# Kernel tuning notes

Hardware: AMD Instinct MI355X
Metric: run time of the kernel (lower is better)

Reference implementation:

```python
import jax, jax.numpy as jnp
import numpy as np

B = 64
BAND = 16384
N_OSC = 32
CH = 64
T_IN = 32
N_NOISE_FRAMES = BAND // 4          # 4096
NOISE_STEP = BAND // N_NOISE_FRAMES  # 4 samples per noise frame
NOISE_COEFFS = NOISE_STEP // 2 + 1   # 3 rfft coefficients
N_UP = int(np.log2(N_NOISE_FRAMES) - np.log2(T_IN))  # 7 doubling blocks
LOWEST_FREQ = 20.0 / 11025.0


def _conv1d(x, w, b, pad):
    # x: (B, Cin, T), w: (Cout, Cin, K)
    out = jax.lax.conv_general_dilated(x, w, (1,), [(pad, pad)],
                                       dimension_numbers=('NCH', 'OIH', 'NCH'))
    return out + b[None, :, None]


def _leaky(x):
    return jnp.where(x > 0, x, 0.2 * x)


def _lin_interp(x, size):
    # torch F.interpolate(mode='linear', align_corners=False) along last axis
    n = x.shape[-1]
    coords = (jnp.arange(size, dtype=jnp.float32) + 0.5) * (n / size) - 0.5
    coords = jnp.clip(coords, 0.0, n - 1.0)
    lo = jnp.floor(coords).astype(jnp.int32)
    hi = jnp.minimum(lo + 1, n - 1)
    frac = (coords - lo.astype(jnp.float32)).astype(x.dtype)
    return x[..., lo] * (1.0 - frac) + x[..., hi] * frac


def setup_inputs() -> dict:
    key = jax.random.key(0)
    ks = jax.random.split(key, 16)
    s = 0.1
    return {
        'x': jax.random.normal(ks[0], (B, T_IN, CH), jnp.float32),
        'noise': jax.random.uniform(ks[1], (B, N_NOISE_FRAMES, NOISE_STEP), jnp.float32, -1.0, 1.0),
        'net_w': jax.random.normal(ks[2], (4, CH, CH, 3), jnp.float32) * s,
        'net_b': jax.random.normal(ks[3], (4, CH), jnp.float32) * s,
        'final_w': jax.random.normal(ks[4], (CH, CH, 3), jnp.float32) * s,
        'final_b': jax.random.normal(ks[5], (CH,), jnp.float32) * s,
        'amp_w': jax.random.normal(ks[6], (N_OSC, CH), jnp.float32) * s,
        'amp_b': jax.random.normal(ks[7], (N_OSC,), jnp.float32) * s,
        'freq_w': jax.random.normal(ks[8], (N_OSC, CH), jnp.float32) * s,
        'freq_b': jax.random.normal(ks[9], (N_OSC,), jnp.float32) * s,
        'nz_init_w': jax.random.normal(ks[10], (CH, CH), jnp.float32) * s,
        'nz_init_b': jax.random.normal(ks[11], (CH,), jnp.float32) * s,
        'nz_up_w': jax.random.normal(ks[12], (N_UP, CH, CH, 3), jnp.float32) * s,
        'nz_up_b': jax.random.normal(ks[13], (N_UP, CH), jnp.float32) * s,
        'nz_final_w': jax.random.normal(ks[14], (NOISE_COEFFS, CH), jnp.float32) * s,
        'nz_final_b': jax.random.normal(ks[15], (NOISE_COEFFS,), jnp.float32) * s,
    }


def reference(x, noise, net_w, net_b, final_w, final_b, amp_w, amp_b, freq_w, freq_b,
              nz_init_w, nz_init_b, nz_up_w, nz_up_b, nz_final_w, nz_final_b):
    z = jnp.transpose(x, (0, 2, 1))  # (B, CH, T_IN)
    for i in range(4):
        z = _leaky(_conv1d(z, net_w[i], net_b[i], 1))
    z = _conv1d(z, final_w, final_b, 1)

    # --- OscillatorBank: sigmoid freq (constrained), abs amp, linear upsample,
    # phase accumulation via cumsum, summed sinusoids ---
    amp = jnp.abs(jnp.einsum('bct,oc->bot', z, amp_w) + amp_b[None, :, None])
    freq = jax.nn.sigmoid(jnp.einsum('bct,oc->bot', z, freq_w) + freq_b[None, :, None])
    freq = LOWEST_FREQ + freq * (1.0 - LOWEST_FREQ)
    amp = _lin_interp(amp, BAND)    # (B, N_OSC, BAND)
    freq = _lin_interp(freq, BAND)  # (B, N_OSC, BAND)
    phase = jnp.cumsum(freq * jnp.pi, axis=-1)
    harm = jnp.sum(amp * jnp.sin(phase), axis=1, keepdims=True)  # (B, 1, BAND)

    # 1x1 conv to rfft coeffs, squared, applied per-frame to uniform noise ---
    y = jnp.einsum('bct,oc->bot', z, nz_init_w) + nz_init_b[None, :, None]
    for i in range(N_UP):
        y = jnp.repeat(y, 2, axis=-1)
        y = _leaky(_conv1d(y, nz_up_w[i], nz_up_b[i], 1))
    coeffs = jnp.einsum('bct,oc->bot', y, nz_final_w) + nz_final_b[None, :, None]
    coeffs = coeffs ** 2                      # squared=True, activation=identity
    coeffs = jnp.transpose(coeffs, (0, 2, 1))  # (B, frames, NOISE_COEFFS)
    spec = jnp.fft.rfft(noise, axis=-1, norm='ortho')   # (B, frames, NOISE_COEFFS)
    filt = spec * coeffs.astype(spec.dtype)
    nz = jnp.fft.irfft(filt, n=NOISE_STEP, axis=-1, norm='ortho')  # (B, frames, step)
    nz = nz.reshape(B, 1, BAND)

    return harm + nz
```

## Files before the change

kernel.cpp:

```cpp
#include <hip/hip_runtime.h>
#include <math.h>

#define LOWEST_FREQ_F 0.00181405895691609977f

typedef short bf16x8 __attribute__((ext_vector_type(8)));
typedef float f32x16 __attribute__((ext_vector_type(16)));

__device__ __forceinline__ float lrelu(float x) { return x > 0.f ? x : 0.2f * x; }
__device__ __forceinline__ float sin_rev(float fr) { return __builtin_amdgcn_sinf(fr); }
__device__ __forceinline__ float bf2f(unsigned short u) {
  union { unsigned int i; float f; } x; x.i = ((unsigned int)u) << 16; return x.f;
}
__device__ __forceinline__ unsigned short f2bf(float f) {
  union { float f; unsigned int i; } x; x.f = f;
  unsigned int r = x.i + 0x7FFFu + ((x.i >> 16) & 1u);
  return (unsigned short)(r >> 16);
}
__device__ __forceinline__ unsigned int pack2(float a, float b) {
  return (unsigned int)f2bf(a) | ((unsigned int)f2bf(b) << 16);
}

__global__ __launch_bounds__(256) void prep_kernel(
    const float* __restrict__ net_w, const float* __restrict__ fin_w,
    const float* __restrict__ amp_w, const float* __restrict__ frq_w,
    const float* __restrict__ nzi_w, const float* __restrict__ nzu_w,
    float* __restrict__ wtF4, float* __restrict__ awfwT,
    float* __restrict__ nzT, short* __restrict__ wfold)
{
  int idx = blockIdx.x * 256 + threadIdx.x;
  if (idx < 20480) {
    int l = idx >> 12, r = idx & 4095;
    int ci = r >> 6, co = r & 63;
    const float* src = (l < 4) ? (net_w + l * 12288) : fin_w;
    const float* wb = src + co * 192 + ci * 3;
    float4 v = make_float4(wb[0], wb[1], wb[2], 0.f);
    ((float4*)wtF4)[idx] = v;
  } else if (idx < 24576) {
    int r = idx - 20480;
    int c2 = r >> 7, rem = r & 127, o = rem >> 2, k = rem & 3;
    int c = c2 * 2 + (k >> 1);
    awfwT[r] = (k & 1) ? frq_w[o * 64 + c] : amp_w[o * 64 + c];
  } else if (idx < 28672) {
    int r = idx - 24576; int c = r >> 6, o = r & 63;
    nzT[r] = nzi_w[o * 64 + c];
  } else if (idx < 28672 + 114688) {
    int r = idx - 28672;
    int l = r >> 14, q = r & 16383;
    int pd = q >> 12, co = (q >> 6) & 63, ci = q & 63;
    const float* wb = nzu_w + l * 12288 + co * 192 + ci * 3;
    float v;
    if      (pd == 0) v = wb[0];
    else if (pd == 1) v = wb[1] + wb[2];
    else if (pd == 2) v = wb[0] + wb[1];
    else              v = wb[2];
    wfold[r] = (short)f2bf(v);
  }
}

template<int TIN>
__device__ __forceinline__ void noise_layer(
    const short* tin, short* tout, const short* __restrict__ wf,
    const float* __restrict__ bias, int tid)
{
  const int L  = tid & 63;
  const int w  = tid >> 6;
  const int mt = w & 1;
  const int ng = w >> 1;

  bf16x8 Af[4][4];
  {
    const short* wb = wf + (mt*32 + (L & 31))*64 + ((L >> 5) << 3);
    #pragma unroll
    for (int pd = 0; pd < 4; ++pd)
      #pragma unroll
      for (int ks = 0; ks < 4; ++ks)
        Af[pd][ks] = *(const bf16x8*)(wb + pd*4096 + ks*16);
  }
  f32x16 binit;
  #pragma unroll
  for (int r = 0; r < 16; ++r)
    binit[r] = bias[mt*32 + (r & 3) + 8*(r >> 2) + 4*(L >> 5)];

  if (tid < 64) { tout[tid] = 0; tout[(2*TIN + 1)*72 + tid] = 0; }

  constexpr int TOT = TIN / 32;
  constexpr int NPG = (TOT + 3) / 4;
  #pragma unroll
  for (int nt = 0; nt < NPG; ++nt) {
    int ntile = ng*NPG + nt;
    if (ntile < TOT) {
      int s = ntile*32 + (L & 31);
      const short* bp = tin + s*72 + ((L >> 5) << 3);
      f32x16 Ce = binit, Co = binit;
      #pragma unroll
      for (int ks = 0; ks < 4; ++ks) {
        bf16x8 Bm = *(const bf16x8*)(bp + ks*16);
        bf16x8 B0 = *(const bf16x8*)(bp + 72 + ks*16);
        bf16x8 Bp = *(const bf16x8*)(bp + 144 + ks*16);
        Ce = __builtin_amdgcn_mfma_f32_32x32x16_bf16(Af[0][ks], Bm, Ce, 0, 0, 0);
        Ce = __builtin_amdgcn_mfma_f32_32x32x16_bf16(Af[1][ks], B0, Ce, 0, 0, 0);
        Co = __builtin_amdgcn_mfma_f32_32x32x16_bf16(Af[2][ks], B0, Co, 0, 0, 0);
        Co = __builtin_amdgcn_mfma_f32_32x32x16_bf16(Af[3][ks], Bp, Co, 0, 0, 0);
      }
      #pragma unroll
      for (int q4 = 0; q4 < 4; ++q4) {
        int co0 = mt*32 + 8*q4 + 4*(L >> 5);
        uint2 ve, vo;
        ve.x = pack2(lrelu(Ce[4*q4+0]), lrelu(Ce[4*q4+1]));
        ve.y = pack2(lrelu(Ce[4*q4+2]), lrelu(Ce[4*q4+3]));
        vo.x = pack2(lrelu(Co[4*q4+0]), lrelu(Co[4*q4+1]));
        vo.y = pack2(lrelu(Co[4*q4+2]), lrelu(Co[4*q4+3]));
        *(uint2*)&tout[(2*s + 1)*72 + co0] = ve;
        *(uint2*)&tout[(2*s + 2)*72 + co0] = vo;
      }
    }
  }
  __syncthreads();
}

template<int NT, int ROFF, bool TOGLOBAL>
__device__ __forceinline__ void up_stage(
    const short* bin, short* bout, unsigned short* gout,
    const short* __restrict__ wf, const float* __restrict__ bias, int tid)
{
  const int L  = tid & 63;
  const int w  = tid >> 6;
  const int mt = w & 1;
  const int pg = w >> 1;

  bf16x8 Af[4][4];
  {
    const short* wb = wf + (mt*32 + (L & 31))*64 + ((L >> 5) << 3);
    #pragma unroll
    for (int pd = 0; pd < 4; ++pd)
      #pragma unroll
      for (int ks = 0; ks < 4; ++ks)
        Af[pd][ks] = *(const bf16x8*)(wb + pd*4096 + ks*16);
  }
  f32x16 binit;
  #pragma unroll
  for (int r = 0; r < 16; ++r)
    binit[r] = bias[mt*32 + (r & 3) + 8*(r >> 2) + 4*(L >> 5)];

  for (int n = pg; n < NT; n += 2) {
    int sl = n*32 + (L & 31);
    const short* bp = bin + (sl + ROFF)*72 + ((L >> 5) << 3);
    f32x16 Ce = binit, Co = binit;
    #pragma unroll
    for (int ks = 0; ks < 4; ++ks) {
      bf16x8 Bm = *(const bf16x8*)(bp + ks*16);
      bf16x8 B0 = *(const bf16x8*)(bp + 72 + ks*16);
      bf16x8 Bp = *(const bf16x8*)(bp + 144 + ks*16);
      Ce = __builtin_amdgcn_mfma_f32_32x32x16_bf16(Af[0][ks], Bm, Ce, 0, 0, 0);
      Ce = __builtin_amdgcn_mfma_f32_32x32x16_bf16(Af[1][ks], B0, Ce, 0, 0, 0);
      Co = __builtin_amdgcn_mfma_f32_32x32x16_bf16(Af[2][ks], B0, Co, 0, 0, 0);
      Co = __builtin_amdgcn_mfma_f32_32x32x16_bf16(Af[3][ks], Bp, Co, 0, 0, 0);
    }
    #pragma unroll
    for (int q4 = 0; q4 < 4; ++q4) {
      int co0 = mt*32 + 8*q4 + 4*(L >> 5);
      uint2 ve, vo;
      ve.x = pack2(lrelu(Ce[4*q4+0]), lrelu(Ce[4*q4+1]));
      ve.y = pack2(lrelu(Ce[4*q4+2]), lrelu(Ce[4*q4+3]));
      vo.x = pack2(lrelu(Co[4*q4+0]), lrelu(Co[4*q4+1]));
      vo.y = pack2(lrelu(Co[4*q4+2]), lrelu(Co[4*q4+3]));
      if (TOGLOBAL) {
        *(uint2*)(gout + (size_t)(2*sl)*64 + co0)     = ve;
        *(uint2*)(gout + (size_t)(2*sl + 1)*64 + co0) = vo;
      } else {
        *(uint2*)&bout[(2*sl)*72 + co0]     = ve;
        *(uint2*)&bout[(2*sl + 1)*72 + co0] = vo;
      }
    }
  }
}

__global__ __launch_bounds__(256) void up345(
    const unsigned short* __restrict__ y3, unsigned short* __restrict__ y6,
    const short* __restrict__ wfold, const float* __restrict__ nzu_b)
{
  __shared__ __align__(16) short s3[66*72];
  __shared__ __align__(16) short s4[128*72];
  __shared__ __align__(16) short s5[192*72];

  const int b   = blockIdx.y;
  const int bx  = blockIdx.x;
  const int tid = threadIdx.x;

  const unsigned short* inb = y3 + (size_t)b * 256 * 64;
  for (int c = tid; c < 66*8; c += 256) {
    int row = c >> 3, pos = (c & 7) << 3;
    int g = 32*bx - 2 + row;
    bf16x8 v = {0,0,0,0,0,0,0,0};
    if (g >= 0 && g < 256) v = *(const bf16x8*)(inb + (size_t)g*64 + pos);
    *(bf16x8*)&s3[row*72 + pos] = v;
  }
  __syncthreads();

  up_stage<2,0,false>(s3, s4, nullptr, wfold + 3*16384, nzu_b + 3*64, tid);
  __syncthreads();
  if (bx == 0) {
    if (tid < 128) s4[(tid >> 6)*72 + (tid & 63)] = 0;
  } else if (bx == 7) {
    for (int i = tid; i < 62*64; i += 256) {
      int r = 66 + (i >> 6);
      s4[r*72 + (i & 63)] = 0;
    }
  }
  __syncthreads();

  up_stage<3,0,false>(s4, s5, nullptr, wfold + 4*16384, nzu_b + 4*64, tid);
  __syncthreads();
  if (bx == 0) {
    if (tid < 128) s5[(tid >> 6)*72 + (tid & 63)] = 0;
  } else if (bx == 7) {
    for (int i = tid; i < 62*64; i += 256) {
      int r = 130 + (i >> 6);
      s5[r*72 + (i & 63)] = 0;
    }
  }
  __syncthreads();

  unsigned short* outb = y6 + ((size_t)b*2048 + 256*bx) * 64;
  up_stage<4,1,true>(s5, nullptr, outb, wfold + 5*16384, nzu_b + 5*64, tid);
}

__global__ __launch_bounds__(512) void z_front(
    const float* __restrict__ x, const float* __restrict__ wtF4,
    const float* __restrict__ net_b, const float* __restrict__ fin_b,
    const float* __restrict__ awfwT, const float* __restrict__ amp_b,
    const float* __restrict__ frq_b,
    const float* __restrict__ nzT, const float* __restrict__ nzi_b,
    const short* __restrict__ wfold, const float* __restrict__ nzu_b,
    unsigned short* __restrict__ y3, float* __restrict__ amp_o,
    float* __restrict__ frq_o, float* __restrict__ ph_o)
{
  __shared__ __align__(16) char arena[86976];
  short* tileB = (short*)arena;
  short* tileA = (short*)(arena + 37152);
  float* za    = (float*)(arena + 55872);
  float* zb    = (float*)(arena + 65088);
  float* zt    = (float*)(arena + 74304);
  float* fl    = (float*)(arena + 82752);

  const int b   = blockIdx.x;
  const int tid = threadIdx.x;
  const int co  = tid & 63;
  const int wv  = tid >> 6;

  for (int idx = tid; idx < 2048; idx += 512) {
    int t = idx >> 6, c = idx & 63;
    za[c*36 + t + 1] = x[b*2048 + idx];
  }
  if (tid < 64) {
    za[tid*36] = 0.f; za[tid*36 + 33] = 0.f;
    zb[tid*36] = 0.f; zb[tid*36 + 33] = 0.f;
  }
  __syncthreads();

  float* pa = za;
  float* pb = zb;
  for (int l = 0; l < 5; ++l) {
    {
      const int t0 = wv << 2;
      float bv = (l < 4) ? net_b[l*64 + co] : fin_b[co];
      float acc[4];
      #pragma unroll
      for (int j = 0; j < 4; ++j) acc[j] = bv;

      const float4* wp = ((const float4*)wtF4) + l*4096 + co;
      float4 wCur[8], wNxt[8];
      #pragma unroll
      for (int k = 0; k < 8; ++k) wCur[k] = wp[k*64];

      for (int cc = 0; cc < 8; ++cc) {
        if (cc < 7) {
          #pragma unroll
          for (int k = 0; k < 8; ++k) wNxt[k] = wp[((cc+1)*8 + k)*64];
        }
        #pragma unroll
        for (int k = 0; k < 8; ++k) {
          const int ci = cc*8 + k;
          const float* rowp = pa + ci*36 + t0;
          float4 zA = *(const float4*)(rowp);
          float2 zB = *(const float2*)(rowp + 4);
          float rr[6] = {zA.x, zA.y, zA.z, zA.w, zB.x, zB.y};
          float4 wgt = wCur[k];
          #pragma unroll
          for (int j = 0; j < 4; ++j) {
            acc[j] = fmaf(wgt.x, rr[j],   acc[j]);
            acc[j] = fmaf(wgt.y, rr[j+1], acc[j]);
            acc[j] = fmaf(wgt.z, rr[j+2], acc[j]);
          }
        }
        if (cc < 7) {
          #pragma unroll
          for (int k = 0; k < 8; ++k) wCur[k] = wNxt[k];
        }
      }

      if (l < 4) {
        #pragma unroll
        for (int j = 0; j < 4; ++j)
          pb[co*36 + t0 + j + 1] = lrelu(acc[j]);
      } else {
        #pragma unroll
        for (int j = 0; j < 4; ++j) {
          int t = t0 + j;
          pb[co*36 + t] = acc[j];
          zt[t*66 + co] = acc[j];
        }
      }
    }
    __syncthreads();
    float* tp = pa; pa = pb; pb = tp;
  }
  const float* zf = pa;

  {
    const int q = wv;
    float bv0 = nzi_b[co];
    float acc[4];
    #pragma unroll
    for (int j = 0; j < 4; ++j) acc[j] = bv0;
    #pragma unroll 8
    for (int c = 0; c < 64; ++c) {
      float4 zv = *(const float4*)(zf + c*36 + (q << 2));
      float wvv = nzT[c*64 + co];
      acc[0] = fmaf(wvv, zv.x, acc[0]);
      acc[1] = fmaf(wvv, zv.y, acc[1]);
      acc[2] = fmaf(wvv, zv.z, acc[2]);
      acc[3] = fmaf(wvv, zv.w, acc[3]);
    }
    #pragma unroll
    for (int j = 0; j < 4; ++j)
      tileA[((q << 2) + j + 1)*72 + co] = (short)f2bf(acc[j]);
  }
  if (tid < 64) { tileA[tid] = 0; tileA[33*72 + tid] = 0; }

  #pragma unroll
  for (int tt = 0; tt < 2; ++tt) {
    int task = tid + 512*tt;
    int o = task & 31, t = task >> 5;
    float aa = amp_b[o], ff = frq_b[o];
    #pragma unroll 8
    for (int c2 = 0; c2 < 32; ++c2) {
      float4 w4 = ((const float4*)awfwT)[c2*32 + o];
      float2 zv = *(const float2*)(zt + t*66 + c2*2);
      aa = fmaf(w4.x, zv.x, aa); ff = fmaf(w4.y, zv.x, ff);
      aa = fmaf(w4.z, zv.y, aa); ff = fmaf(w4.w, zv.y, ff);
    }
    aa = fabsf(aa);
    float sg = 1.f / (1.f + expf(-ff));
    float fq = LOWEST_FREQ_F + sg * (1.f - LOWEST_FREQ_F);
    amp_o[b*1024 + o*32 + t] = aa;
    frq_o[b*1024 + o*32 + t] = fq;
    fl[o*33 + t] = fq;
  }
  __syncthreads();

  if (wv == 7 && (tid & 63) < 32) {
    const int o = tid & 31;
    double P = 256.0 * (double)fl[o*33];
    double hd = P * 0.5;
    ph_o[b*1024 + o*32] = (float)(hd - floor(hd));
    for (int i = 1; i < 32; ++i) {
      P += 256.0 * ((double)fl[o*33 + i - 1] + (double)fl[o*33 + i]);
      hd = P * 0.5;
      ph_o[b*1024 + o*32 + i] = (float)(hd - floor(hd));
    }
  }

  noise_layer<32> (tileA, tileB, wfold + 0*16384, nzu_b + 0*64, tid);
  noise_layer<64> (tileB, tileA, wfold + 1*16384, nzu_b + 1*64, tid);
  noise_layer<128>(tileA, tileB, wfold + 2*16384, nzu_b + 2*64, tid);

  unsigned short* yb = y3 + (size_t)b * 16384;
  for (int c = tid; c < 2048; c += 512) {
    int row = c >> 3, pos = (c & 7) << 3;
    *(bf16x8*)(yb + c*8) = *(const bf16x8*)&tileB[(row + 1)*72 + pos];
  }
}

__global__ __launch_bounds__(256) void final_fused(
    const unsigned short* __restrict__ in,
    const short* __restrict__ wf, const float* __restrict__ bias,
    const float* __restrict__ nzf_w, const float* __restrict__ nzf_b,
    const float* __restrict__ noise,
    const float* __restrict__ amp, const float* __restrict__ frq,
    const float* __restrict__ ph, float* __restrict__ out)
{
  constexpr int STILE = 128, Tin = 2048, ROWS = STILE + 2, G = STILE / 64;
  __shared__ __align__(16) short lB[ROWS * 72];
  __shared__ __align__(16) short yT[256 * 72];
  __shared__ float al[1024], fqv[1024], pl[1024];
  __shared__ float wl[192];

  const int b   = blockIdx.y;
  const int s0  = blockIdx.x * STILE;
  const int tid = threadIdx.x;
  const int L   = tid & 63;
  const int w   = tid >> 6;
  const int mt  = w & 1;
  const int ng  = w >> 1;

  for (int i = tid; i < 1024; i += 256) {
    al[i]  = amp[b*1024 + i];
    fqv[i] = frq[b*1024 + i];
    pl[i]  = ph[b*1024 + i];
  }
  if (tid < 192) { int o = tid >> 6, c = tid & 63; wl[c*3 + o] = nzf_w[tid]; }

  bf16x8 Af[4][4];
  {
    const short* wb = wf + (mt*32 + (L & 31))*64 + ((L >> 5) << 3);
    #pragma unroll
    for (int pd = 0; pd < 4; ++pd)
      #pragma unroll
      for (int ks = 0; ks < 4; ++ks)
        Af[pd][ks] = *(const bf16x8*)(wb + pd*4096 + ks*16);
  }

  const unsigned short* inb = in + (size_t)b * Tin * 64;
  for (int c = tid; c < ROWS*8; c += 256) {
    int row = c >> 3, pos = (c & 7) << 3;
    int g = s0 - 1 + row;
    bf16x8 v = {0,0,0,0,0,0,0,0};
    if (g >= 0 && g < Tin) v = *(const bf16x8*)(inb + (size_t)g*64 + pos);
    *(bf16x8*)&lB[row*72 + pos] = v;
  }

  f32x16 binit;
  #pragma unroll
  for (int r = 0; r < 16; ++r)
    binit[r] = bias[mt*32 + (r & 3) + 8*(r >> 2) + 4*(L >> 5)];

  __syncthreads();

  #pragma unroll
  for (int nt = 0; nt < G; ++nt) {
    int s_loc = ng*(32*G) + nt*32 + (L & 31);
    const short* bp = lB + s_loc*72 + ((L >> 5) << 3);
    f32x16 Ce = binit, Co = binit;
    #pragma unroll
    for (int ks = 0; ks < 4; ++ks) {
      bf16x8 Bm = *(const bf16x8*)(bp + ks*16);
      bf16x8 B0 = *(const bf16x8*)(bp + 72 + ks*16);
      bf16x8 Bp = *(const bf16x8*)(bp + 144 + ks*16);
      Ce = __builtin_amdgcn_mfma_f32_32x32x16_bf16(Af[0][ks], Bm, Ce, 0, 0, 0);
      Ce = __builtin_amdgcn_mfma_f32_32x32x16_bf16(Af[1][ks], B0, Ce, 0, 0, 0);
      Co = __builtin_amdgcn_mfma_f32_32x32x16_bf16(Af[2][ks], B0, Co, 0, 0, 0);
      Co = __builtin_amdgcn_mfma_f32_32x32x16_bf16(Af[3][ks], Bp, Co, 0, 0, 0);
    }
    #pragma unroll
    for (int q4 = 0; q4 < 4; ++q4) {
      int co0 = mt*32 + 8*q4 + 4*(L >> 5);
      uint2 ve, vo;
      ve.x = pack2(lrelu(Ce[4*q4+0]), lrelu(Ce[4*q4+1]));
      ve.y = pack2(lrelu(Ce[4*q4+2]), lrelu(Ce[4*q4+3]));
      vo.x = pack2(lrelu(Co[4*q4+0]), lrelu(Co[4*q4+1]));
      vo.y = pack2(lrelu(Co[4*q4+2]), lrelu(Co[4*q4+3]));
      *(uint2*)&yT[(2*s_loc)*72 + co0]     = ve;
      *(uint2*)&yT[(2*s_loc + 1)*72 + co0] = vo;
    }
  }
  __syncthreads();

  {
    const short* yr = &yT[tid * 72];
    float c0 = nzf_b[0], c1 = nzf_b[1], c2 = nzf_b[2];
    #pragma unroll
    for (int c8 = 0; c8 < 8; ++c8) {
      bf16x8 v = *(const bf16x8*)(yr + c8*8);
      #pragma unroll
      for (int j = 0; j < 8; ++j) {
        float yv = bf2f((unsigned short)v[j]);
        int c = c8*8 + j;
        c0 = fmaf(wl[c*3+0], yv, c0);
        c1 = fmaf(wl[c*3+1], yv, c1);
        c2 = fmaf(wl[c*3+2], yv, c2);
      }
    }
    c0 *= c0; c1 *= c1; c2 *= c2;

    const int fb = 2*s0 + tid;
    const float4 n = *(const float4*)(noise + ((size_t)b*4096 + fb)*4);
    float F0  = c0 * (n.x + n.y + n.z + n.w) * 0.5f;
    float F1r = c1 * (n.x - n.z) * 0.5f;
    float F1i = -(c1 * (n.y - n.w) * 0.5f);
    float F2  = c2 * (n.x - n.y + n.z - n.w) * 0.5f;
    float r0 = 0.5f * (F0 + 2.f*F1r + F2);
    float r1 = 0.5f * (F0 - 2.f*F1i - F2);
    float r2 = 0.5f * (F0 - 2.f*F1r + F2);
    float r3 = 0.5f * (F0 + 2.f*F1i - F2);

    const int t0 = fb * 4;
    float s0a = 0.f, s1a = 0.f, s2a = 0.f, s3a = 0.f;
    if (t0 < 256) {
      const float tp = (float)(t0 + 1) * 0.5f;
      #pragma unroll 4
      for (int o = 0; o < 32; ++o) {
        float f0 = fqv[o*32], am = al[o*32];
        float hf = 0.5f * f0;
        float v0 = tp * f0, v1 = v0 + hf, v2 = v1 + hf, v3 = v2 + hf;
        s0a += am * sin_rev(v0 - floorf(v0));
        s1a += am * sin_rev(v1 - floorf(v1));
        s2a += am * sin_rev(v2 - floorf(v2));
        s3a += am * sin_rev(v3 - floorf(v3));
      }
    } else if (t0 >= 16128) {
      const float tp = (float)(t0 - 16127) * 0.5f;
      #pragma unroll 4
      for (int o = 0; o < 32; ++o) {
        float f0 = fqv[o*32 + 31], am = al[o*32 + 31], p = pl[o*32 + 31];
        float hf = 0.5f * f0;
        float v0 = p + tp * f0, v1 = v0 + hf, v2 = v1 + hf, v3 = v2 + hf;
        s0a += am * sin_rev(v0 - floorf(v0));
        s1a += am * sin_rev(v1 - floorf(v1));
        s2a += am * sin_rev(v2 - floorf(v2));
        s3a += am * sin_rev(v3 - floorf(v3));
      }
    } else {
      const int i  = (t0 - 256) >> 9;
      const int m0 = (t0 - 256) & 511;
      float mm[4], fa[4], mq[4];
      #pragma unroll
      for (int js = 0; js < 4; ++js) {
        float mmv = (float)(m0 + 1 + js);
        mm[js] = mmv;
        fa[js] = ((float)(m0 + js) + 0.5f) * (1.f/512.f);
        mq[js] = mmv * mmv * (1.f/1024.f);
      }
      #pragma unroll 4
      for (int o = 0; o < 32; ++o) {
        float f0 = fqv[o*32 + i], f1 = fqv[o*32 + i + 1];
        float a0 = al[o*32 + i],  a1 = al[o*32 + i + 1];
        float p  = pl[o*32 + i];
        float df = f1 - f0, da = a1 - a0;
        #pragma unroll
        for (int js = 0; js < 4; ++js) {
          float av   = fmaf(da, fa[js], a0);
          float part = fmaf(df, mq[js], mm[js] * f0);
          float v    = fmaf(part, 0.5f, p);
          float fr   = v - floorf(v);
          float sv   = av * sin_rev(fr);
          if      (js == 0) s0a += sv;
          else if (js == 1) s1a += sv;
          else if (js == 2) s2a += sv;
          else              s3a += sv;
        }
      }
    }
    float4 res = make_float4(s0a + r0, s1a + r1, s2a + r2, s3a + r3);
    *(float4*)(out + ((size_t)b*4096 + fb)*4) = res;
  }
}

extern "C" void kernel_launch(void* const* d_in, const int* in_sizes, int n_in,
                              void* d_out, int out_size, void* d_ws, size_t ws_size,
                              hipStream_t stream) {
  (void)in_sizes; (void)n_in; (void)out_size; (void)ws_size;
  const float* x     = (const float*)d_in[0];
  const float* noise = (const float*)d_in[1];
  const float* net_w = (const float*)d_in[2];
  const float* net_b = (const float*)d_in[3];
  const float* fin_w = (const float*)d_in[4];
  const float* fin_b = (const float*)d_in[5];
  const float* amp_w = (const float*)d_in[6];
  const float* amp_b = (const float*)d_in[7];
  const float* frq_w = (const float*)d_in[8];
  const float* frq_b = (const float*)d_in[9];
  const float* nzi_w = (const float*)d_in[10];
  const float* nzi_b = (const float*)d_in[11];
  const float* nzu_w = (const float*)d_in[12];
  const float* nzu_b = (const float*)d_in[13];
  const float* nzf_w = (const float*)d_in[14];
  const float* nzf_b = (const float*)d_in[15];
  float* out = (float*)d_out;

  short* y3    = (short*)d_ws;
  short* y6    = y3 + (size_t)64*256*64;
  short* wfold = y6 + (size_t)64*2048*64;
  float* wtF4  = (float*)(wfold + 7*16384);
  float* awfwT = wtF4 + 81920;
  float* nzT   = awfwT + 4096;
  float* ampv  = nzT + 4096;
  float* frqv  = ampv + 65536;
  float* phv   = frqv + 65536;

  prep_kernel<<<dim3(560), dim3(256), 0, stream>>>(
      net_w, fin_w, amp_w, frq_w, nzi_w, nzu_w, wtF4, awfwT, nzT, wfold);

  z_front<<<dim3(64), dim3(512), 0, stream>>>(
      x, wtF4, net_b, fin_b, awfwT, amp_b, frq_b, nzT, nzi_b,
      wfold, nzu_b, (unsigned short*)y3, ampv, frqv, phv);

  up345<<<dim3(8, 64), dim3(256), 0, stream>>>(
      (unsigned short*)y3, (unsigned short*)y6, wfold, nzu_b);

  final_fused<<<dim3(16, 64), dim3(256), 0, stream>>>(
      (unsigned short*)y6, wfold + 6*16384, nzu_b + 6*64,
      nzf_w, nzf_b, noise, ampv, frqv, phv, out);
}
```

Baseline: 204.7 us.

## Double z_front threads and split conv input channels across waves

z_front now launches 1024 threads per block instead of 512. The five conv layers are restructured so that each thread handles one time step and 8 output channels over a slice of input channels. Partial sums are reduced with a cross-half shuffle plus an LDS scratch buffer and an extra barrier. The noise init, amp/freq projection and noise_layer tile distribution (NPG halved) are adjusted to the larger block, aiming to cut the latency of this 64-block, underoccupied kernel at the cost of more LDS, reduction overhead and register pressure under 1024-thread bounds.

```diff
diff --git a/kernel.cpp b/kernel.cpp
--- a/kernel.cpp
+++ b/kernel.cpp
@@ -84,7 +84,7 @@
   if (tid < 64) { tout[tid] = 0; tout[(2*TIN + 1)*72 + tid] = 0; }
 
   constexpr int TOT = TIN / 32;
-  constexpr int NPG = (TOT + 3) / 4;
+  constexpr int NPG = (TOT + 7) / 8;
   #pragma unroll
   for (int nt = 0; nt < NPG; ++nt) {
     int ntile = ng*NPG + nt;
@@ -225,7 +225,7 @@
   up_stage<4,1,true>(s5, nullptr, outb, wfold + 5*16384, nzu_b + 5*64, tid);
 }
 
-__global__ __launch_bounds__(512) void z_front(
+__global__ __launch_bounds__(1024) void z_front(
     const float* __restrict__ x, const float* __restrict__ wtF4,
     const float* __restrict__ net_b, const float* __restrict__ fin_b,
     const float* __restrict__ awfwT, const float* __restrict__ amp_b,
@@ -235,20 +235,21 @@
     unsigned short* __restrict__ y3, float* __restrict__ amp_o,
     float* __restrict__ frq_o, float* __restrict__ ph_o)
 {
-  __shared__ __align__(16) char arena[86976];
+  __shared__ __align__(16) char arena[95168];
   short* tileB = (short*)arena;
   short* tileA = (short*)(arena + 37152);
   float* za    = (float*)(arena + 55872);
   float* zb    = (float*)(arena + 65088);
   float* zt    = (float*)(arena + 74304);
   float* fl    = (float*)(arena + 82752);
+  float* sc    = (float*)(arena + 86976);
 
   const int b   = blockIdx.x;
   const int tid = threadIdx.x;
   const int co  = tid & 63;
   const int wv  = tid >> 6;
 
-  for (int idx = tid; idx < 2048; idx += 512) {
+  for (int idx = tid; idx < 2048; idx += 1024) {
     int t = idx >> 6, c = idx & 63;
     za[c*36 + t + 1] = x[b*2048 + idx];
   }
@@ -258,57 +259,81 @@
   }
   __syncthreads();
 
+  const int L    = tid & 63;
+  const int t    = L & 31;
+  const int half = L >> 5;
+  const int co8  = wv & 7;
+  const int ciq  = wv >> 3;
+
   float* pa = za;
   float* pb = zb;
   for (int l = 0; l < 5; ++l) {
+    float acc[8];
+    if (ciq == 0 && half == 0) {
+      const float* bp = (l < 4) ? (net_b + l*64) : fin_b;
+      #pragma unroll
+      for (int j = 0; j < 8; ++j) acc[j] = bp[co8*8 + j];
+    } else {
+      #pragma unroll
+      for (int j = 0; j < 8; ++j) acc[j] = 0.f;
+    }
+
+    const float4* wp = ((const float4*)wtF4) + l*4096 + co8*8;
+    const int ci0 = ciq*32 + half;
+
+    float4 wc[8];
+    float zc0, zc1, zc2;
     {
-      const int t0 = wv << 2;
-      float bv = (l < 4) ? net_b[l*64 + co] : fin_b[co];
-      float acc[4];
-      #pragma unroll
-      for (int j = 0; j < 4; ++j) acc[j] = bv;
-
-      const float4* wp = ((const float4*)wtF4) + l*4096 + co;
-      float4 wCur[8], wNxt[8];
-      #pragma unroll
-      for (int k = 0; k < 8; ++k) wCur[k] = wp[k*64];
-
-      for (int cc = 0; cc < 8; ++cc) {
-        if (cc < 7) {
-          #pragma unroll
-          for (int k = 0; k < 8; ++k) wNxt[k] = wp[((cc+1)*8 + k)*64];
-        }
+      const float* zr = pa + ci0*36 + t;
+      zc0 = zr[0]; zc1 = zr[1]; zc2 = zr[2];
+      #pragma unroll
+      for (int j = 0; j < 8; ++j) wc[j] = wp[ci0*64 + j];
+    }
+    #pragma unroll
+    for (int s = 0; s < 16; ++s) {
+      float4 wn[8];
+      float zn0 = 0.f, zn1 = 0.f, zn2 = 0.f;
+      if (s < 15) {
+        int ci = ci0 + 2*(s + 1);
+        const float* zr = pa + ci*36 + t;
+        zn0 = zr[0]; zn1 = zr[1]; zn2 = zr[2];
         #pragma unroll
-        for (int k = 0; k < 8; ++k) {
-          const int ci = cc*8 + k;
-          const float* rowp = pa + ci*36 + t0;
-          float4 zA = *(const float4*)(rowp);
-          float2 zB = *(const float2*)(rowp + 4);
-          float rr[6] = {zA.x, zA.y, zA.z, zA.w, zB.x, zB.y};
-          float4 wgt = wCur[k];
-          #pragma unroll
-          for (int j = 0; j < 4; ++j) {
-            acc[j] = fmaf(wgt.x, rr[j],   acc[j]);
-            acc[j] = fmaf(wgt.y, rr[j+1], acc[j]);
-            acc[j] = fmaf(wgt.z, rr[j+2], acc[j]);
-          }
-        }
-        if (cc < 7) {
-          #pragma unroll
-          for (int k = 0; k < 8; ++k) wCur[k] = wNxt[k];
-        }
-      }
-
-      if (l < 4) {
+        for (int j = 0; j < 8; ++j) wn[j] = wp[ci*64 + j];
+      }
+      #pragma unroll
+      for (int j = 0; j < 8; ++j) {
+        acc[j] = fmaf(wc[j].x, zc0, acc[j]);
+        acc[j] = fmaf(wc[j].y, zc1, acc[j]);
+        acc[j] = fmaf(wc[j].z, zc2, acc[j]);
+      }
+      if (s < 15) {
+        zc0 = zn0; zc1 = zn1; zc2 = zn2;
         #pragma unroll
-        for (int j = 0; j < 4; ++j)
-          pb[co*36 + t0 + j + 1] = lrelu(acc[j]);
-      } else {
-        #pragma unroll
-        for (int j = 0; j < 4; ++j) {
-          int t = t0 + j;
-          pb[co*36 + t] = acc[j];
-          zt[t*66 + co] = acc[j];
+        for (int j = 0; j < 8; ++j) wc[j] = wn[j];
+      }
+    }
+    #pragma unroll
+    for (int j = 0; j < 8; ++j) acc[j] += __shfl_xor(acc[j], 32, 64);
+
+    if (ciq == 1) {
+      #pragma unroll
+      for (int jj = 0; jj < 4; ++jj) {
+        int j = half*4 + jj;
+        sc[(co8*8 + j)*32 + t] = acc[j];
+      }
+    }
+    __syncthreads();
+    if (ciq == 0) {
+      #pragma unroll
+      for (int jj = 0; jj < 4; ++jj) {
+        int j = half*4 + jj;
+        int c = co8*8 + j;
+        float v = acc[j] + sc[c*32 + t];
+        if (l < 4) {
+          pb[c*36 + t + 1] = lrelu(v);
+        } else {
+          pb[c*36 + t] = v;
+          zt[t*66 + c] = v;
         }
       }
     }
@@ -318,48 +343,41 @@
   const float* zf = pa;
 
   {
-    const int q = wv;
+    const int t0 = wv*2;
     float bv0 = nzi_b[co];
-    float acc[4];
-    #pragma unroll
-    for (int j = 0; j < 4; ++j) acc[j] = bv0;
+    float acc0 = bv0, acc1 = bv0;
     #pragma unroll 8
     for (int c = 0; c < 64; ++c) {
-      float4 zv = *(const float4*)(zf + c*36 + (q << 2));
+      float2 zv = *(const float2*)(zf + c*36 + t0);
       float wvv = nzT[c*64 + co];
-      acc[0] = fmaf(wvv, zv.x, acc[0]);
-      acc[1] = fmaf(wvv, zv.y, acc[1]);
-      acc[2] = fmaf(wvv, zv.z, acc[2]);
-      acc[3] = fmaf(wvv, zv.w, acc[3]);
-    }
-    #pragma unroll
-    for (int j = 0; j < 4; ++j)
-      tileA[((q << 2) + j + 1)*72 + co] = (short)f2bf(acc[j]);
+      acc0 = fmaf(wvv, zv.x, acc0);
+      acc1 = fmaf(wvv, zv.y, acc1);
+    }
+    tileA[(t0 + 1)*72 + co] = (short)f2bf(acc0);
+    tileA[(t0 + 2)*72 + co] = (short)f2bf(acc1);
   }
   if (tid < 64) { tileA[tid] = 0; tileA[33*72 + tid] = 0; }
 
-  #pragma unroll
-  for (int tt = 0; tt < 2; ++tt) {
-    int task = tid + 512*tt;
-    int o = task & 31, t = task >> 5;
+  {
+    int o = tid & 31, tt = tid >> 5;
     float aa = amp_b[o], ff = frq_b[o];
     #pragma unroll 8
     for (int c2 = 0; c2 < 32; ++c2) {
       float4 w4 = ((const float4*)awfwT)[c2*32 + o];
-      float2 zv = *(const float2*)(zt + t*66 + c2*2);
+      float2 zv = *(const float2*)(zt + tt*66 + c2*2);
       aa = fmaf(w4.x, zv.x, aa); ff = fmaf(w4.y, zv.x, ff);
       aa = fmaf(w4.z, zv.y, aa); ff = fmaf(w4.w, zv.y, ff);
     }
     aa = fabsf(aa);
     float sg = 1.f / (1.f + expf(-ff));
     float fq = LOWEST_FREQ_F + sg * (1.f - LOWEST_FREQ_F);
-    amp_o[b*1024 + o*32 + t] = aa;
-    frq_o[b*1024 + o*32 + t] = fq;
-    fl[o*33 + t] = fq;
-  }
-  __syncthreads();
-
-  if (wv == 7 && (tid & 63) < 32) {
+    amp_o[b*1024 + o*32 + tt] = aa;
+    frq_o[b*1024 + o*32 + tt] = fq;
+    fl[o*33 + tt] = fq;
+  }
+  __syncthreads();
+
+  if (wv == 15 && (tid & 63) < 32) {
     const int o = tid & 31;
     double P = 256.0 * (double)fl[o*33];
     double hd = P * 0.5;
@@ -376,7 +394,7 @@
   noise_layer<128>(tileA, tileB, wfold + 2*16384, nzu_b + 2*64, tid);
 
   unsigned short* yb = y3 + (size_t)b * 16384;
-  for (int c = tid; c < 2048; c += 512) {
+  for (int c = tid; c < 2048; c += 1024) {
     int row = c >> 3, pos = (c & 7) << 3;
     *(bf16x8*)(yb + c*8) = *(const bf16x8*)&tileB[(row + 1)*72 + pos];
   }
@@ -591,7 +609,7 @@
   prep_kernel<<<dim3(560), dim3(256), 0, stream>>>(
       net_w, fin_w, amp_w, frq_w, nzi_w, nzu_w, wtF4, awfwT, nzT, wfold);
 
-  z_front<<<dim3(64), dim3(512), 0, stream>>>(
+  z_front<<<dim3(64), dim3(1024), 0, stream>>>(
       x, wtF4, net_b, fin_b, awfwT, amp_b, frq_b, nzT, nzi_b,
       wfold, nzu_b, (unsigned short*)y3, ampv, frqv, phv);
 
```

Measured after the change: 295.1 us. 44.2% more time.
